# Kernel tuning notes

Measured on AMD Instinct MI355X. Metric: run time of the kernel, lower is better.

Reference implementation:

```python
import jax, jax.numpy as jnp
import numpy as np

B, L, V, H, NL = 128, 512, 2048, 512, 2


def setup_inputs() -> dict:
    key = jax.random.key(0)
    ks = jax.random.split(key, 20)
    s = 0.05  # param scale
    inp = {
        "input_ids": jax.random.randint(ks[0], (B,), 0, V),
        "last_hidden": jax.random.normal(ks[1], (NL, B, H), jnp.float32),
        "word_dict_vec": jax.random.normal(ks[2], (B, V, H), jnp.float32),
        "encoder_outputs": jax.random.normal(ks[3], (L, B, H), jnp.float32),
        "seq_mask": (jax.random.uniform(ks[4], (B, L)) < 0.2).at[:, 0].set(False),
        # Attn params (torch Linear: y = x @ W.T + b)
        "attn_W": jax.random.normal(ks[5], (H, 2 * H), jnp.float32) * s,
        "attn_b": jax.random.normal(ks[6], (H,), jnp.float32) * s,
        "score_W": jax.random.normal(ks[7], (1, H), jnp.float32) * s,
        # concat layer
        "concat_W": jax.random.normal(ks[8], (H, 2 * H), jnp.float32) * s,
        "concat_b": jax.random.normal(ks[9], (H,), jnp.float32) * s,
        # GRU layer 0 (input 2H) and layer 1 (input H); gates ordered r,z,n as in torch
        "W_ih0": jax.random.normal(ks[10], (3 * H, 2 * H), jnp.float32) * s,
        "W_hh0": jax.random.normal(ks[11], (3 * H, H), jnp.float32) * s,
        "b_ih0": jax.random.normal(ks[12], (3 * H,), jnp.float32) * s,
        "b_hh0": jax.random.normal(ks[13], (3 * H,), jnp.float32) * s,
        "W_ih1": jax.random.normal(ks[14], (3 * H, H), jnp.float32) * s,
        "W_hh1": jax.random.normal(ks[15], (3 * H, H), jnp.float32) * s,
        "b_ih1": jax.random.normal(ks[16], (3 * H,), jnp.float32) * s,
        "b_hh1": jax.random.normal(ks[17], (3 * H,), jnp.float32) * s,
    }
    return inp


def _gru_cell(x, h, W_ih, W_hh, b_ih, b_hh):
    gi = x @ W_ih.T + b_ih
    gh = h @ W_hh.T + b_hh
    i_r, i_z, i_n = jnp.split(gi, 3, axis=-1)
    h_r, h_z, h_n = jnp.split(gh, 3, axis=-1)
    r = jax.nn.sigmoid(i_r + h_r)
    z = jax.nn.sigmoid(i_z + h_z)
    n = jnp.tanh(i_n + r * h_n)
    return (1.0 - z) * n + z * h


def reference(input_ids, last_hidden, word_dict_vec, encoder_outputs, seq_mask,
              attn_W, attn_b, score_W, concat_W, concat_b,
              W_ih0, W_hh0, b_ih0, b_hh0, W_ih1, W_hh1, b_ih1, b_hh1):
    # one_hot @ word_dict_vec == per-batch row gather (same math)
    emb = word_dict_vec[jnp.arange(B), input_ids]  # [B, H]

    # Bahdanau additive attention over encoder_outputs [L, B, H]
    q = last_hidden[-1]  # [B, H]
    hid = jnp.broadcast_to(q[None], (L, B, H))
    energy_in = jnp.concatenate([hid, encoder_outputs], axis=2)  # [L, B, 2H]
    e = jnp.tanh(energy_in @ attn_W.T + attn_b) @ score_W.T      # [L, B, 1]
    scores = e[..., 0].T                                          # [B, L]
    scores = jnp.where(seq_mask, jnp.float32(-1e12), scores)
    aw = jax.nn.softmax(scores, axis=1)                           # [B, L]

    context = jnp.einsum('bl,lbh->bh', aw, encoder_outputs)       # [B, H]

    # single-step 2-layer GRU (eval mode: dropout = identity)
    x0 = jnp.concatenate([emb, context], axis=1)                  # [B, 2H]
    h0 = _gru_cell(x0, last_hidden[0], W_ih0, W_hh0, b_ih0, b_hh0)
    h1 = _gru_cell(h0, last_hidden[1], W_ih1, W_hh1, b_ih1, b_hh1)
    hidden = jnp.stack([h0, h1])                                  # [2, B, H]

    output = jnp.tanh(jnp.concatenate([h1, context], axis=1) @ concat_W.T + concat_b)
    return output, hidden
```

## Files before the change

### kernel.cpp

```cpp
#include <hip/hip_runtime.h>
#include <stdint.h>

#define Hdim 512
#define Bdim 128
#define Ldim 512
#define Vdim 2048

typedef unsigned short u16;
using f32x4  = float  __attribute__((ext_vector_type(4)));
using bf16x8 = __bf16 __attribute__((ext_vector_type(8)));

__device__ inline u16 f2bf(float x) {
  uint32_t u = __float_as_uint(x);
  u += 0x7fffu + ((u >> 16) & 1u);
  return (u16)(u >> 16);
}
__device__ inline uint32_t pk2(float lo, float hi) {
  return (uint32_t)f2bf(lo) | ((uint32_t)f2bf(hi) << 16);
}
__device__ inline float fast_tanh(float x) {
  return 1.0f - 2.0f / (__expf(2.0f * x) + 1.0f);
}
__device__ inline float fast_sig(float x) { return 1.0f / (1.0f + __expf(-x)); }

__device__ inline bf16x8 pack_bf8(float4 x, float4 y) {
  union { uint32_t d[4]; bf16x8 v; } r;
  r.d[0] = pk2(x.x, x.y); r.d[1] = pk2(x.z, x.w);
  r.d[2] = pk2(y.x, y.y); r.d[3] = pk2(y.z, y.w);
  return r.v;
}

__global__ __launch_bounds__(512)
void prep_kernel(const float* __restrict__ lh, const float* __restrict__ attn_W,
                 const float* __restrict__ attn_b, const float* __restrict__ cat_W,
                 const float* __restrict__ W_ih0, const float* __restrict__ W_hh0,
                 const float* __restrict__ W_ih1, const float* __restrict__ W_hh1,
                 const float* __restrict__ b_ih0, const float* __restrict__ b_hh0,
                 const float* __restrict__ b_ih1, const float* __restrict__ b_hh1,
                 const float* __restrict__ wdv, const int* __restrict__ ids,
                 const void* __restrict__ mask,
                 float* __restrict__ qW, u16* __restrict__ arena,
                 float* __restrict__ biasg0, float* __restrict__ biasg1,
                 u16* __restrict__ X0bf, u16* __restrict__ X1bf, int* __restrict__ flag) {
  int blk = blockIdx.x, t = threadIdx.x;
  int lane = t & 63, wid = t >> 6;
  int fr = lane & 15, g = lane >> 4, kof = g * 8;

  if (blk < 16) {
    int mh = wid & 3, nh = wid >> 2;
    int n0 = blk * 32 + nh * 16;
    int rb0 = mh * 32;
    f32x4 ac0 = {0.f, 0.f, 0.f, 0.f}, ac1 = {0.f, 0.f, 0.f, 0.f};
    const float* q = lh + 65536;
#pragma unroll 2
    for (int kt = 0; kt < 512; kt += 32) {
      const float* qr0 = q + (size_t)(rb0 + fr) * 512 + kt + kof;
      const float* qr1 = qr0 + 16 * 512;
      const float* wr  = attn_W + (size_t)(n0 + fr) * 1024 + kt + kof;
      float4 x0 = *(const float4*)qr0, x1 = *(const float4*)(qr0 + 4);
      float4 y0 = *(const float4*)qr1, y1 = *(const float4*)(qr1 + 4);
      float4 w0 = *(const float4*)wr,  w1 = *(const float4*)(wr + 4);
      bf16x8 A0 = pack_bf8(x0, x1), A1 = pack_bf8(y0, y1), Bb = pack_bf8(w0, w1);
      ac0 = __builtin_amdgcn_mfma_f32_16x16x32_bf16(A0, Bb, ac0, 0, 0, 0);
      ac1 = __builtin_amdgcn_mfma_f32_16x16x32_bf16(A1, Bb, ac1, 0, 0, 0);
    }
    float vb = attn_b[n0 + fr];
#pragma unroll
    for (int j = 0; j < 4; ++j) {
      qW[(size_t)(rb0 + g * 4 + j) * 512 + n0 + fr]      = ac0[j] + vb;
      qW[(size_t)(rb0 + 16 + g * 4 + j) * 512 + n0 + fr] = ac1[j] + vb;
    }
    return;
  }
  if (blk == 16) {
    __shared__ int sf;
    if (t == 0) sf = 0;
    __syncthreads();
    const uint32_t* m32 = (const uint32_t*)mask;
    int found = 0;
    for (int i = t; i < 16384; i += 512)
      if (m32[i] & 0xffffff00u) found = 1;
    if (found) sf = 1;
    __syncthreads();
    if (t == 0) *flag = sf;
    return;
  }
  const int ARENA_Q = 1507328;
  int i = (blk - 17) * 512 + t;
  if (i < ARENA_Q) {
    int e = i * 4;
    float4 v = {0.f, 0.f, 0.f, 0.f};
    if (e < 262144) {
      int o = e >> 9, k = e & 511;
      v = *(const float4*)(attn_W + (size_t)o * 1024 + 512 + k);
    } else if (e < 786432) {
      int e2 = e - 262144; int o = e2 >> 10, k = e2 & 1023;
      v = *(const float4*)(cat_W + (size_t)o * 1024 + k);
    } else if (e < 3932160) {
      int e2 = e - 786432; int row = e2 / 1536, k = e2 % 1536;
      int o = row >> 2, gt = row & 3;
      if (gt == 0)      v = (k < 1024) ? *(const float4*)(W_ih0 + (size_t)o * 1024 + k)
                                       : *(const float4*)(W_hh0 + (size_t)o * 512 + k - 1024);
      else if (gt == 1) v = (k < 1024) ? *(const float4*)(W_ih0 + (size_t)(512 + o) * 1024 + k)
                                       : *(const float4*)(W_hh0 + (size_t)(512 + o) * 512 + k - 1024);
      else if (gt == 2) { if (k < 1024)  v = *(const float4*)(W_ih0 + (size_t)(1024 + o) * 1024 + k); }
      else              { if (k >= 1024) v = *(const float4*)(W_hh0 + (size_t)(1024 + o) * 512 + k - 1024); }
    } else {
      int e2 = e - 3932160; int row = e2 >> 10, k = e2 & 1023;
      int o = row >> 2, gt = row & 3;
      if (gt == 0)      v = (k < 512) ? *(const float4*)(W_ih1 + (size_t)o * 512 + k)
                                      : *(const float4*)(W_hh1 + (size_t)o * 512 + k - 512);
      else if (gt == 1) v = (k < 512) ? *(const float4*)(W_ih1 + (size_t)(512 + o) * 512 + k)
                                      : *(const float4*)(W_hh1 + (size_t)(512 + o) * 512 + k - 512);
      else if (gt == 2) { if (k < 512)  v = *(const float4*)(W_ih1 + (size_t)(1024 + o) * 512 + k); }
      else              { if (k >= 512) v = *(const float4*)(W_hh1 + (size_t)(1024 + o) * 512 + k - 512); }
    }
    ushort4 u;
    u.x = f2bf(v.x); u.y = f2bf(v.y); u.z = f2bf(v.z); u.w = f2bf(v.w);
    *(ushort4*)(arena + e) = u;
    return;
  }
  int i2 = i - ARENA_Q;
  if (i2 < 1024) {
    int r4 = i2 * 4; int layer = r4 >> 11; int r = r4 & 2047; int o = r >> 2;
    const float* bi = layer ? b_ih1 : b_ih0;
    const float* bh = layer ? b_hh1 : b_hh0;
    float4 v;
    v.x = bi[o] + bh[o];
    v.y = bi[512 + o] + bh[512 + o];
    v.z = bi[1024 + o];
    v.w = bh[1024 + o];
    *(float4*)((layer ? biasg1 : biasg0) + r) = v;
  } else if (i2 < 1024 + 16384) {
    int j = (i2 - 1024) * 4; int b = j >> 9, i0 = j & 511;
    float4 v = *(const float4*)(wdv + (size_t)b * (Vdim * Hdim) + (size_t)ids[b] * 512 + i0);
    ushort4 u;
    u.x = f2bf(v.x); u.y = f2bf(v.y); u.z = f2bf(v.z); u.w = f2bf(v.w);
    *(ushort4*)(X0bf + b * 1536 + i0) = u;
  } else if (i2 < 1024 + 32768) {
    int j = (i2 - 1024 - 16384) * 4; int b = j >> 9, i0 = j & 511;
    float4 v = *(const float4*)(lh + (size_t)b * 512 + i0);
    ushort4 u;
    u.x = f2bf(v.x); u.y = f2bf(v.y); u.z = f2bf(v.z); u.w = f2bf(v.w);
    *(ushort4*)(X0bf + b * 1536 + 1024 + i0) = u;
  } else if (i2 < 1024 + 49152) {
    int j = (i2 - 1024 - 32768) * 4; int b = j >> 9, i0 = j & 511;
    float4 v = *(const float4*)(lh + 65536 + (size_t)b * 512 + i0);
    ushort4 u;
    u.x = f2bf(v.x); u.y = f2bf(v.y); u.z = f2bf(v.z); u.w = f2bf(v.w);
    *(ushort4*)(X1bf + b * 1024 + 512 + i0) = u;
  }
}

__global__ __launch_bounds__(512)
void attn_kernel(const float* __restrict__ enc, const u16* __restrict__ Wenc,
                 const float* __restrict__ qW, const float* __restrict__ scW,
                 float* __restrict__ scores_p) {
  __shared__ __align__(16) u16 As[2][128 * 40];
  __shared__ __align__(16) u16 Bs[2][256 * 40];
  __shared__ float part[8 * 128];
  int blk = blockIdx.x, t = threadIdx.x;
  int lane = t & 63, wid = t >> 6;
  int fr = lane & 15, g = lane >> 4, kof = g * 8;
  int l  = (blk >> 4) * 8 + (blk & 7);
  int oh = (blk >> 3) & 1;
  int ob = oh * 256;
  const int arow = t >> 2;
  const int aks = (t & 3) * 8;

  f32x4 acc[8][2];
#pragma unroll
  for (int i = 0; i < 8; ++i) {
    acc[i][0] = (f32x4){0.f, 0.f, 0.f, 0.f};
    acc[i][1] = (f32x4){0.f, 0.f, 0.f, 0.f};
  }
  const float* abase = enc + ((size_t)l * 128 + arow) * 512 + aks;
  const u16* bbase0 = Wenc + (size_t)(ob + arow) * 512 + aks;
  const u16* bbase1 = bbase0 + (size_t)128 * 512;

  float4 ra0 = *(const float4*)abase;
  float4 ra1 = *(const float4*)(abase + 4);
  uint4 rb0 = *(const uint4*)bbase0;
  uint4 rb1 = *(const uint4*)bbase1;

#pragma unroll 2
  for (int step = 0; step < 16; ++step) {
    int sel = step & 1;
    __syncthreads();
    uint4 ap;
    ap.x = pk2(ra0.x, ra0.y); ap.y = pk2(ra0.z, ra0.w);
    ap.z = pk2(ra1.x, ra1.y); ap.w = pk2(ra1.z, ra1.w);
    *(uint4*)(&As[sel][arow * 40 + aks]) = ap;
    *(uint4*)(&Bs[sel][arow * 40 + aks]) = rb0;
    *(uint4*)(&Bs[sel][(128 + arow) * 40 + aks]) = rb1;
    if (step < 15) {
      int kt = (step + 1) * 32;
      ra0 = *(const float4*)(abase + kt);
      ra1 = *(const float4*)(abase + kt + 4);
      rb0 = *(const uint4*)(bbase0 + kt);
      rb1 = *(const uint4*)(bbase1 + kt);
    }
    __syncthreads();
    bf16x8 b0 = *(const bf16x8*)(&Bs[sel][(wid * 32 + fr) * 40 + kof]);
    bf16x8 b1 = *(const bf16x8*)(&Bs[sel][(wid * 32 + 16 + fr) * 40 + kof]);
#pragma unroll
    for (int mi = 0; mi < 8; ++mi) {
      bf16x8 av = *(const bf16x8*)(&As[sel][(mi * 16 + fr) * 40 + kof]);
      acc[mi][0] = __builtin_amdgcn_mfma_f32_16x16x32_bf16(av, b0, acc[mi][0], 0, 0, 0);
      acc[mi][1] = __builtin_amdgcn_mfma_f32_16x16x32_bf16(av, b1, acc[mi][1], 0, 0, 0);
    }
  }
#pragma unroll
  for (int mi = 0; mi < 8; ++mi) {
    float rs0 = 0.f, rs1 = 0.f, rs2 = 0.f, rs3 = 0.f;
#pragma unroll
    for (int ni = 0; ni < 2; ++ni) {
      int o = ob + wid * 32 + ni * 16 + fr;
      float sw = scW[o];
      int brow = mi * 16 + g * 4;
      rs0 += sw * fast_tanh(acc[mi][ni][0] + qW[(size_t)(brow + 0) * 512 + o]);
      rs1 += sw * fast_tanh(acc[mi][ni][1] + qW[(size_t)(brow + 1) * 512 + o]);
      rs2 += sw * fast_tanh(acc[mi][ni][2] + qW[(size_t)(brow + 2) * 512 + o]);
      rs3 += sw * fast_tanh(acc[mi][ni][3] + qW[(size_t)(brow + 3) * 512 + o]);
    }
#pragma unroll
    for (int d = 1; d < 16; d <<= 1) {
      rs0 += __shfl_xor(rs0, d);
      rs1 += __shfl_xor(rs1, d);
      rs2 += __shfl_xor(rs2, d);
      rs3 += __shfl_xor(rs3, d);
    }
    if (fr < 4) {
      float v = (fr == 0) ? rs0 : (fr == 1) ? rs1 : (fr == 2) ? rs2 : rs3;
      part[wid * 128 + mi * 16 + g * 4 + fr] = v;
    }
  }
  __syncthreads();
  if (t < 128) {
    float s = 0.f;
#pragma unroll
    for (int w2 = 0; w2 < 8; ++w2) s += part[w2 * 128 + t];
    scores_p[(size_t)(oh * 128 + t) * 512 + l] = s;
  }
}

__global__ __launch_bounds__(256)
void softctx_kernel(const float* __restrict__ sp, const void* __restrict__ maskp,
                    const int* __restrict__ flag, const float* __restrict__ enc,
                    u16* __restrict__ X0bf, u16* __restrict__ c1bf) {
  int bx = blockIdx.x;
  int b = bx >> 2, c = bx & 3;
  int t = threadIdx.x;
  __shared__ float wgt[512];
  __shared__ float redm[4], reds[4];
  __shared__ float ps[4][64][2];
  int l0 = t, l1 = t + 256;
  float s0 = sp[(size_t)b * 512 + l0] + sp[(size_t)(128 + b) * 512 + l0];
  float s1 = sp[(size_t)b * 512 + l1] + sp[(size_t)(128 + b) * 512 + l1];
  bool isbyte = (*flag != 0);
  bool m0, m1;
  if (isbyte) {
    m0 = ((const uint8_t*)maskp)[b * 512 + l0] != 0;
    m1 = ((const uint8_t*)maskp)[b * 512 + l1] != 0;
  } else {
    m0 = ((const int*)maskp)[b * 512 + l0] != 0;
    m1 = ((const int*)maskp)[b * 512 + l1] != 0;
  }
  float v0 = m0 ? -1e12f : s0;
  float v1 = m1 ? -1e12f : s1;
  float mx = fmaxf(v0, v1);
#pragma unroll
  for (int d = 1; d < 64; d <<= 1) mx = fmaxf(mx, __shfl_xor(mx, d));
  if ((t & 63) == 0) redm[t >> 6] = mx;
  __syncthreads();
  mx = fmaxf(fmaxf(redm[0], redm[1]), fmaxf(redm[2], redm[3]));
  float e0 = __expf(v0 - mx), e1 = __expf(v1 - mx);
  float sm = e0 + e1;
#pragma unroll
  for (int d = 1; d < 64; d <<= 1) sm += __shfl_xor(sm, d);
  if ((t & 63) == 0) reds[t >> 6] = sm;
  __syncthreads();
  sm = reds[0] + reds[1] + reds[2] + reds[3];
  float inv = 1.0f / sm;
  wgt[l0] = e0 * inv;
  wgt[l1] = e1 * inv;
  __syncthreads();
  int cp = t & 63, lq = t >> 6;
  int col = c * 128 + cp * 2;
  float a0 = 0.f, a1 = 0.f;
  for (int l = lq * 128; l < lq * 128 + 128; ++l) {
    float wl = wgt[l];
    if (wl != 0.0f) {
      float2 ev = *(const float2*)(enc + ((size_t)l * 128 + b) * 512 + col);
      a0 += wl * ev.x;
      a1 += wl * ev.y;
    }
  }
  ps[lq][cp][0] = a0;
  ps[lq][cp][1] = a1;
  __syncthreads();
  if (t < 64) {
    float r0 = ps[0][t][0] + ps[1][t][0] + ps[2][t][0] + ps[3][t][0];
    float r1 = ps[0][t][1] + ps[1][t][1] + ps[2][t][1] + ps[3][t][1];
    int cc = c * 128 + t * 2;
    uint32_t packed = pk2(r0, r1);
    *(uint32_t*)(X0bf + b * 1536 + 512 + cc) = packed;
    *(uint32_t*)(c1bf + b * 1024 + 512 + cc) = packed;
  }
}

__global__ __launch_bounds__(256)
void gru_gemm_kernel(const u16* __restrict__ X, int ldx, const u16* __restrict__ Wp,
                     const float* __restrict__ biasp, const float* __restrict__ hprev,
                     int K, float* __restrict__ hout, u16* __restrict__ xdst) {
  __shared__ float ct[128][36];
  int n0 = blockIdx.x * 32;
  int t = threadIdx.x, lane = t & 63, w = t >> 6;
  int fr = lane & 15, g = lane >> 4, kof = g * 8;
  f32x4 acc[2][2];
#pragma unroll
  for (int i = 0; i < 2; ++i)
#pragma unroll
    for (int j = 0; j < 2; ++j) acc[i][j] = (f32x4){0.f, 0.f, 0.f, 0.f};
  const u16* Xr0 = X + (size_t)(w * 32 + fr) * ldx;
  const u16* Xr1 = Xr0 + (size_t)16 * ldx;
  const u16* Wr0 = Wp + (size_t)(n0 + fr) * K;
  const u16* Wr1 = Wp + (size_t)(n0 + 16 + fr) * K;
#pragma unroll 4
  for (int kt = 0; kt < K; kt += 32) {
    bf16x8 a0 = *(const bf16x8*)(Xr0 + kt + kof);
    bf16x8 a1 = *(const bf16x8*)(Xr1 + kt + kof);
    bf16x8 b0 = *(const bf16x8*)(Wr0 + kt + kof);
    bf16x8 b1 = *(const bf16x8*)(Wr1 + kt + kof);
    acc[0][0] = __builtin_amdgcn_mfma_f32_16x16x32_bf16(a0, b0, acc[0][0], 0, 0, 0);
    acc[0][1] = __builtin_amdgcn_mfma_f32_16x16x32_bf16(a0, b1, acc[0][1], 0, 0, 0);
    acc[1][0] = __builtin_amdgcn_mfma_f32_16x16x32_bf16(a1, b0, acc[1][0], 0, 0, 0);
    acc[1][1] = __builtin_amdgcn_mfma_f32_16x16x32_bf16(a1, b1, acc[1][1], 0, 0, 0);
  }
#pragma unroll
  for (int mi = 0; mi < 2; ++mi)
#pragma unroll
    for (int ni = 0; ni < 2; ++ni) {
      int col = ni * 16 + fr;
      float vb = biasp[n0 + col];
#pragma unroll
      for (int j = 0; j < 4; ++j)
        ct[w * 32 + 16 * mi + g * 4 + j][col] = acc[mi][ni][j] + vb;
    }
  __syncthreads();
#pragma unroll
  for (int i = 0; i < 4; ++i) {
    int u = t + i * 256;
    int b = u >> 3, ol = u & 7;
    float cr  = ct[b][ol * 4 + 0];
    float cz  = ct[b][ol * 4 + 1];
    float ci  = ct[b][ol * 4 + 2];
    float chh = ct[b][ol * 4 + 3];
    int o = blockIdx.x * 8 + ol;
    float r = fast_sig(cr), z = fast_sig(cz);
    float n = tanhf(ci + r * chh);
    float h = (1.0f - z) * n + z * hprev[b * 512 + o];
    hout[b * 512 + o] = h;
    xdst[b * 1024 + o] = f2bf(h);
  }
}

__global__ __launch_bounds__(256)
void thin_gemm32(const u16* __restrict__ X, int ldx, const u16* __restrict__ W,
                 const float* __restrict__ bias, float* __restrict__ C, int ldc,
                 int K, int act) {
  int n0 = blockIdx.x * 32;
  int t = threadIdx.x, lane = t & 63, w = t >> 6;
  int fr = lane & 15, g = lane >> 4, kof = g * 8;
  f32x4 acc[2][2];
#pragma unroll
  for (int i = 0; i < 2; ++i)
#pragma unroll
    for (int j = 0; j < 2; ++j) acc[i][j] = (f32x4){0.f, 0.f, 0.f, 0.f};
  const u16* Xr0 = X + (size_t)(w * 32 + fr) * ldx;
  const u16* Xr1 = Xr0 + (size_t)16 * ldx;
  const u16* Wr0 = W + (size_t)(n0 + fr) * K;
  const u16* Wr1 = W + (size_t)(n0 + 16 + fr) * K;
#pragma unroll 4
  for (int kt = 0; kt < K; kt += 32) {
    bf16x8 a0 = *(const bf16x8*)(Xr0 + kt + kof);
    bf16x8 a1 = *(const bf16x8*)(Xr1 + kt + kof);
    bf16x8 b0 = *(const bf16x8*)(Wr0 + kt + kof);
    bf16x8 b1 = *(const bf16x8*)(Wr1 + kt + kof);
    acc[0][0] = __builtin_amdgcn_mfma_f32_16x16x32_bf16(a0, b0, acc[0][0], 0, 0, 0);
    acc[0][1] = __builtin_amdgcn_mfma_f32_16x16x32_bf16(a0, b1, acc[0][1], 0, 0, 0);
    acc[1][0] = __builtin_amdgcn_mfma_f32_16x16x32_bf16(a1, b0, acc[1][0], 0, 0, 0);
    acc[1][1] = __builtin_amdgcn_mfma_f32_16x16x32_bf16(a1, b1, acc[1][1], 0, 0, 0);
  }
#pragma unroll
  for (int mi = 0; mi < 2; ++mi)
#pragma unroll
    for (int ni = 0; ni < 2; ++ni) {
      int col = n0 + ni * 16 + fr;
      float vb = bias[col];
#pragma unroll
      for (int j = 0; j < 4; ++j) {
        int row = w * 32 + 16 * mi + g * 4 + j;
        float v = acc[mi][ni][j] + vb;
        if (act) v = tanhf(v);
        C[(size_t)row * ldc + col] = v;
      }
    }
}

extern "C" void kernel_launch(void* const* d_in, const int* in_sizes, int n_in,
                              void* d_out, int out_size, void* d_ws, size_t ws_size,
                              hipStream_t stream) {
  const int*   ids    = (const int*)  d_in[0];
  const float* lh     = (const float*)d_in[1];
  const float* wdv    = (const float*)d_in[2];
  const float* enc    = (const float*)d_in[3];
  const void*  mask   = d_in[4];
  const float* attn_W = (const float*)d_in[5];
  const float* attn_b = (const float*)d_in[6];
  const float* scW    = (const float*)d_in[7];
  const float* cat_W  = (const float*)d_in[8];
  const float* cat_b  = (const float*)d_in[9];
  const float* W_ih0  = (const float*)d_in[10];
  const float* W_hh0  = (const float*)d_in[11];
  const float* b_ih0  = (const float*)d_in[12];
  const float* b_hh0  = (const float*)d_in[13];
  const float* W_ih1  = (const float*)d_in[14];
  const float* W_hh1  = (const float*)d_in[15];
  const float* b_ih1  = (const float*)d_in[16];
  const float* b_hh1  = (const float*)d_in[17];

  float* out = (float*)d_out;
  float* h0  = out + 65536;
  float* h1  = out + 131072;

  float* ws       = (float*)d_ws;
  float* qW       = ws;
  float* scores_p = ws + 65536;
  float* biasg0   = ws + 196608;
  float* biasg1   = ws + 198656;
  int*   flag     = (int*)(ws + 200704);
  u16*   arena    = (u16*)(ws + 200720);
  u16*   X0bf     = (u16*)(ws + 3215376);
  u16*   X1bf     = (u16*)(ws + 3313680);
  u16*   c1bf     = (u16*)(ws + 3379216);

  const u16* Wenc = arena;
  const u16* Wcat = arena + 262144;
  const u16* Wg0p = arena + 786432;
  const u16* Wg1p = arena + 3932160;

  prep_kernel<<<3059, 512, 0, stream>>>(lh, attn_W, attn_b, cat_W,
                                        W_ih0, W_hh0, W_ih1, W_hh1,
                                        b_ih0, b_hh0, b_ih1, b_hh1,
                                        wdv, ids, mask,
                                        qW, arena, biasg0, biasg1, X0bf, X1bf, flag);
  attn_kernel<<<1024, 512, 0, stream>>>(enc, Wenc, qW, scW, scores_p);
  softctx_kernel<<<512, 256, 0, stream>>>(scores_p, mask, flag, enc, X0bf, c1bf);
  gru_gemm_kernel<<<64, 256, 0, stream>>>(X0bf, 1536, Wg0p, biasg0, lh, 1536, h0, X1bf);
  gru_gemm_kernel<<<64, 256, 0, stream>>>(X1bf, 1024, Wg1p, biasg1, lh + 65536, 1024, h1, c1bf);
  thin_gemm32<<<16, 256, 0, stream>>>(c1bf, 1024, Wcat, cat_b, out, 512, 1024, 1);
}
```

Before: 187.8 us.

## Load attention weights directly into registers and widen context kernel parallelism

In attn_kernel, the Wenc B-tile is no longer staged through shared memory. Each wave loads its MFMA B-fragment straight from global memory into registers and prefetches one step ahead, which cuts LDS traffic and shared memory use per block. softctx_kernel now runs 1024 blocks, each covering 64 columns with 8 L-slices, and drops the skip on zero weights so the loop can unroll and pipeline its loads. The trade-off is redundant global reads of Wenc across waves and reading encoder rows even where the mask zeroes the weight.

```diff
diff --git a/kernel.cpp b/kernel.cpp
--- a/kernel.cpp
+++ b/kernel.cpp
@@ -157,7 +157,6 @@
                  const float* __restrict__ qW, const float* __restrict__ scW,
                  float* __restrict__ scores_p) {
   __shared__ __align__(16) u16 As[2][128 * 40];
-  __shared__ __align__(16) u16 Bs[2][256 * 40];
   __shared__ float part[8 * 128];
   int blk = blockIdx.x, t = threadIdx.x;
   int lane = t & 63, wid = t >> 6;
@@ -175,13 +174,13 @@
     acc[i][1] = (f32x4){0.f, 0.f, 0.f, 0.f};
   }
   const float* abase = enc + ((size_t)l * 128 + arow) * 512 + aks;
-  const u16* bbase0 = Wenc + (size_t)(ob + arow) * 512 + aks;
-  const u16* bbase1 = bbase0 + (size_t)128 * 512;
+  const u16* bptr0 = Wenc + (size_t)(ob + wid * 32 + fr) * 512 + kof;
+  const u16* bptr1 = bptr0 + (size_t)16 * 512;
 
   float4 ra0 = *(const float4*)abase;
   float4 ra1 = *(const float4*)(abase + 4);
-  uint4 rb0 = *(const uint4*)bbase0;
-  uint4 rb1 = *(const uint4*)bbase1;
+  bf16x8 cb0 = *(const bf16x8*)bptr0;
+  bf16x8 cb1 = *(const bf16x8*)bptr1;
 
 #pragma unroll 2
   for (int step = 0; step < 16; ++step) {
@@ -191,24 +190,22 @@
     ap.x = pk2(ra0.x, ra0.y); ap.y = pk2(ra0.z, ra0.w);
     ap.z = pk2(ra1.x, ra1.y); ap.w = pk2(ra1.z, ra1.w);
     *(uint4*)(&As[sel][arow * 40 + aks]) = ap;
-    *(uint4*)(&Bs[sel][arow * 40 + aks]) = rb0;
-    *(uint4*)(&Bs[sel][(128 + arow) * 40 + aks]) = rb1;
+    bf16x8 nb0 = cb0, nb1 = cb1;
     if (step < 15) {
       int kt = (step + 1) * 32;
       ra0 = *(const float4*)(abase + kt);
       ra1 = *(const float4*)(abase + kt + 4);
-      rb0 = *(const uint4*)(bbase0 + kt);
-      rb1 = *(const uint4*)(bbase1 + kt);
+      nb0 = *(const bf16x8*)(bptr0 + kt);
+      nb1 = *(const bf16x8*)(bptr1 + kt);
     }
     __syncthreads();
-    bf16x8 b0 = *(const bf16x8*)(&Bs[sel][(wid * 32 + fr) * 40 + kof]);
-    bf16x8 b1 = *(const bf16x8*)(&Bs[sel][(wid * 32 + 16 + fr) * 40 + kof]);
 #pragma unroll
     for (int mi = 0; mi < 8; ++mi) {
       bf16x8 av = *(const bf16x8*)(&As[sel][(mi * 16 + fr) * 40 + kof]);
-      acc[mi][0] = __builtin_amdgcn_mfma_f32_16x16x32_bf16(av, b0, acc[mi][0], 0, 0, 0);
-      acc[mi][1] = __builtin_amdgcn_mfma_f32_16x16x32_bf16(av, b1, acc[mi][1], 0, 0, 0);
-    }
+      acc[mi][0] = __builtin_amdgcn_mfma_f32_16x16x32_bf16(av, cb0, acc[mi][0], 0, 0, 0);
+      acc[mi][1] = __builtin_amdgcn_mfma_f32_16x16x32_bf16(av, cb1, acc[mi][1], 0, 0, 0);
+    }
+    cb0 = nb0; cb1 = nb1;
   }
 #pragma unroll
   for (int mi = 0; mi < 8; ++mi) {
@@ -248,12 +245,12 @@
 void softctx_kernel(const float* __restrict__ sp, const void* __restrict__ maskp,
                     const int* __restrict__ flag, const float* __restrict__ enc,
                     u16* __restrict__ X0bf, u16* __restrict__ c1bf) {
-  int bx = blockIdx.x;
-  int b = bx >> 2, c = bx & 3;
-  int t = threadIdx.x;
   __shared__ float wgt[512];
   __shared__ float redm[4], reds[4];
-  __shared__ float ps[4][64][2];
+  __shared__ float ps[256 * 2];
+  int blk = blockIdx.x, t = threadIdx.x;
+  int lane = t & 63, wid = t >> 6;
+  int b = blk >> 3, c = blk & 7;
   int l0 = t, l1 = t + 256;
   float s0 = sp[(size_t)b * 512 + l0] + sp[(size_t)(128 + b) * 512 + l0];
   float s1 = sp[(size_t)b * 512 + l1] + sp[(size_t)(128 + b) * 512 + l1];
@@ -271,38 +268,42 @@
   float mx = fmaxf(v0, v1);
 #pragma unroll
   for (int d = 1; d < 64; d <<= 1) mx = fmaxf(mx, __shfl_xor(mx, d));
-  if ((t & 63) == 0) redm[t >> 6] = mx;
+  if (lane == 0) redm[wid] = mx;
   __syncthreads();
   mx = fmaxf(fmaxf(redm[0], redm[1]), fmaxf(redm[2], redm[3]));
   float e0 = __expf(v0 - mx), e1 = __expf(v1 - mx);
   float sm = e0 + e1;
 #pragma unroll
   for (int d = 1; d < 64; d <<= 1) sm += __shfl_xor(sm, d);
-  if ((t & 63) == 0) reds[t >> 6] = sm;
+  if (lane == 0) reds[wid] = sm;
   __syncthreads();
   sm = reds[0] + reds[1] + reds[2] + reds[3];
   float inv = 1.0f / sm;
   wgt[l0] = e0 * inv;
   wgt[l1] = e1 * inv;
   __syncthreads();
-  int cp = t & 63, lq = t >> 6;
-  int col = c * 128 + cp * 2;
+  int cp = t & 31, lq = t >> 5;
+  int col = c * 64 + cp * 2;
   float a0 = 0.f, a1 = 0.f;
-  for (int l = lq * 128; l < lq * 128 + 128; ++l) {
-    float wl = wgt[l];
-    if (wl != 0.0f) {
-      float2 ev = *(const float2*)(enc + ((size_t)l * 128 + b) * 512 + col);
-      a0 += wl * ev.x;
-      a1 += wl * ev.y;
-    }
-  }
-  ps[lq][cp][0] = a0;
-  ps[lq][cp][1] = a1;
-  __syncthreads();
-  if (t < 64) {
-    float r0 = ps[0][t][0] + ps[1][t][0] + ps[2][t][0] + ps[3][t][0];
-    float r1 = ps[0][t][1] + ps[1][t][1] + ps[2][t][1] + ps[3][t][1];
-    int cc = c * 128 + t * 2;
+  const float* ebase = enc + (size_t)b * 512 + col;
+#pragma unroll 4
+  for (int l2 = lq * 64; l2 < lq * 64 + 64; ++l2) {
+    float wl = wgt[l2];
+    float2 ev = *(const float2*)(ebase + (size_t)l2 * 65536);
+    a0 += wl * ev.x;
+    a1 += wl * ev.y;
+  }
+  ps[(lq * 32 + cp) * 2 + 0] = a0;
+  ps[(lq * 32 + cp) * 2 + 1] = a1;
+  __syncthreads();
+  if (t < 32) {
+    float r0 = 0.f, r1 = 0.f;
+#pragma unroll
+    for (int q2 = 0; q2 < 8; ++q2) {
+      r0 += ps[(q2 * 32 + t) * 2 + 0];
+      r1 += ps[(q2 * 32 + t) * 2 + 1];
+    }
+    int cc = c * 64 + t * 2;
     uint32_t packed = pk2(r0, r1);
     *(uint32_t*)(X0bf + b * 1536 + 512 + cc) = packed;
     *(uint32_t*)(c1bf + b * 1024 + 512 + cc) = packed;
@@ -456,7 +457,7 @@
                                         wdv, ids, mask,
                                         qW, arena, biasg0, biasg1, X0bf, X1bf, flag);
   attn_kernel<<<1024, 512, 0, stream>>>(enc, Wenc, qW, scW, scores_p);
-  softctx_kernel<<<512, 256, 0, stream>>>(scores_p, mask, flag, enc, X0bf, c1bf);
+  softctx_kernel<<<1024, 256, 0, stream>>>(scores_p, mask, flag, enc, X0bf, c1bf);
   gru_gemm_kernel<<<64, 256, 0, stream>>>(X0bf, 1536, Wg0p, biasg0, lh, 1536, h0, X1bf);
   gru_gemm_kernel<<<64, 256, 0, stream>>>(X1bf, 1024, Wg1p, biasg1, lh + 65536, 1024, h1, c1bf);
   thin_gemm32<<<16, 256, 0, stream>>>(c1bf, 1024, Wcat, cat_b, out, 512, 1024, 1);
```

Measured after the change: 173.0 us. 1.09x faster.
